# Performance work log

Measured on AMD Instinct MI355X. Metric: run time of the kernel, lower is better.

## Reference

```python
import jax, jax.numpy as jnp
import numpy as np

PILLAR_WH = np.array([0.16, 0.16], np.float32)
MAX_POINTS = 100
MAX_PILLARS = 12000
MIN_XYZ = np.array([-51.2, -51.2, -5.0], np.float32)
MAX_XYZ = np.array([51.2, 51.2, 3.0], np.float32)
PAD_VALUE = 0.0
NGRID = np.ceil((MAX_XYZ[:2] - MIN_XYZ[:2]) / PILLAR_WH).astype(np.int32)  # [640, 640]
WH_N = (2.0 * PILLAR_WH / (MAX_XYZ[:2] - MIN_XYZ[:2])).astype(np.float32)  # pillar size in normalized coords
MIN_XY_N = (MIN_XYZ[:2] / MAX_XYZ[:2]).astype(np.float32)  # = [-1, -1]


def setup_inputs() -> dict:
    key = jax.random.key(0)
    B, P = 4, 50000
    k1, k2, k3 = jax.random.split(key, 3)
    # x,y restricted to [-8, 8] m so occupied pillars (<=100x100=10000) <= max_pillars,
    # making the torch module's random pillar subsampling a deterministic no-op.
    xy = jax.random.uniform(k1, (B, P, 2), minval=-8.0, maxval=8.0, dtype=jnp.float32)
    z = jax.random.uniform(k2, (B, P, 1), minval=-5.0, maxval=3.0, dtype=jnp.float32)
    r = jax.random.uniform(k3, (B, P, 1), dtype=jnp.float32)
    return {"point_clouds": jnp.concatenate([xy, z, r], axis=-1)}


def _per_sample(pc, pidx):
    # pc: (P, 4) normalized points; pidx: (P,) int32 pillar ids
    P = pc.shape[0]
    u, inv = jnp.unique(pidx, size=MAX_PILLARS, fill_value=-1, return_inverse=True)
    counts = jax.ops.segment_sum(jnp.ones((P,), jnp.int32), inv, num_segments=MAX_PILLARS)
    sums = jax.ops.segment_sum(pc[:, :3], inv, num_segments=MAX_PILLARS)
    mean = sums / jnp.maximum(counts, 1).astype(pc.dtype)[:, None]
    # stable sort points by pillar id; rank = position within pillar
    order = jnp.argsort(inv)
    seg = inv[order]
    pts = pc[order]
    start = jnp.cumsum(counts) - counts  # exclusive prefix of counts
    rank = jnp.arange(P, dtype=jnp.int32) - start[seg]
    in_cap = rank < MAX_POINTS
    flat = jnp.where(in_cap, seg * MAX_POINTS + rank, MAX_PILLARS * MAX_POINTS)  # OOB -> dropped
    buf = jnp.zeros((MAX_PILLARS * MAX_POINTS, 4), pc.dtype).at[flat].set(pts, mode='drop')
    occ = jnp.zeros((MAX_PILLARS * MAX_POINTS,), bool).at[flat].set(True, mode='drop')
    buf = buf.reshape(MAX_PILLARS, MAX_POINTS, 4)
    occ = occ.reshape(MAX_PILLARS, MAX_POINTS)
    ij = jnp.stack([u % NGRID[0], u // NGRID[0]], axis=-1).astype(pc.dtype)
    centers = jnp.asarray(MIN_XY_N) + ij * jnp.asarray(WH_N) + jnp.asarray(WH_N) * 0.5
    feat_c = jnp.abs(buf[..., :3] - mean[:, None, :])  # |xyz - pillar mean|
    feat_p = centers[:, None, :] - buf[..., :2]        # pillar center offset
    out = jnp.concatenate([buf, feat_c, feat_p], axis=-1)  # (max_pillars, max_points, 9)
    out = jnp.where(occ[..., None], out, jnp.asarray(PAD_VALUE, pc.dtype))
    return out, u


def reference(point_clouds):
    pc = point_clouds
    xyz_n = 2.0 * (pc[..., :3] - jnp.asarray(MIN_XYZ)) / jnp.asarray(MAX_XYZ - MIN_XYZ) - 1.0
    pc_n = jnp.concatenate([xyz_n, pc[..., 3:]], axis=-1)
    ij = jnp.minimum(
        jnp.floor((xyz_n[..., :2] - jnp.asarray(MIN_XY_N)) / jnp.asarray(WH_N)),
        jnp.asarray(NGRID, xyz_n.dtype) - 1.0,
    ).astype(jnp.int32)
    pidx = ij[..., 1] * int(NGRID[0]) + ij[..., 0]
    out, pillars = jax.vmap(_per_sample)(pc_n, pidx)
    return out, pillars
```

## Files before the change

### kernel.cpp

```cpp
#include <hip/hip_runtime.h>

#define NB 4
#define GRID_X 640
#define NCELL (GRID_X*GRID_X)
#define NWORD (NCELL/32)
#define MAXPIL 12000
#define MAXPTS 100
#define NBLKA (NWORD/256)

typedef unsigned short u16;
typedef unsigned int   u32;

__device__ __forceinline__ float bf16rt(float f) {
    u32 u = __builtin_bit_cast(u32, f);
    u32 r = ((u + 0x7FFFu + ((u >> 16) & 1u)) >> 16) << 16;
    return __builtin_bit_cast(float, r);
}

__device__ __forceinline__ float opaquef(float x) { asm volatile("" : "+v"(x)); return x; }

#define R102 0.009765625f
#define RWH  320.000030517578125f
__device__ __host__ constexpr float WH_N_C() { return (2.0f*0.16f)/(51.2f-(-51.2f)); }

__device__ __forceinline__ float norm_x(float v) {
    float p = 2.0f*(v + 51.2f) * R102;
    return opaquef(p) - 1.0f;
}
__device__ __forceinline__ float norm_z(float v) {
    float p = 2.0f*(v + 5.0f) * 0.125f;
    return opaquef(p) - 1.0f;
}

__device__ __forceinline__ int cell_of(float xn, float yn) {
    float fx = fminf(fmaxf(floorf((xn + 1.0f) * RWH), 0.0f), 639.0f);
    float fy = fminf(fmaxf(floorf((yn + 1.0f) * RWH), 0.0f), 639.0f);
    return (int)fy * GRID_X + (int)fx;
}

__global__ void k_init(int4* __restrict__ ws4, int nw4,
                       float* __restrict__ pillars_f, int* __restrict__ slotCell, int npil) {
    int i = blockIdx.x*blockDim.x + threadIdx.x;
    if (i < nw4) ws4[i] = make_int4(0,0,0,0);
    if (i < npil) { pillars_f[i] = -1.0f; slotCell[i] = -1; }
}

__global__ void k_mask(const float4* __restrict__ pc, int P,
                       u32* __restrict__ occMask, u32* __restrict__ pidxBuf) {
    int i = blockIdx.x*blockDim.x + threadIdx.x;
    if (i >= NB*P) return;
    float4 pt = pc[i];
    int cell = cell_of(norm_x(pt.x), norm_x(pt.y));
    int b = i / P;
    atomicOr(&occMask[b*NWORD + (cell >> 5)], 1u << (cell & 31));
    pidxBuf[i] = (u32)cell;
}

__global__ void k_scanA(const u32* __restrict__ occMask, int* __restrict__ blockSums) {
    __shared__ int lds[256];
    int blk = blockIdx.x % NBLKA;
    int b   = blockIdx.x / NBLKA;
    int w   = blk*256 + threadIdx.x;
    lds[threadIdx.x] = __popc(occMask[b*NWORD + w]);
    __syncthreads();
    for (int d = 128; d > 0; d >>= 1) {
        if (threadIdx.x < d) lds[threadIdx.x] += lds[threadIdx.x + d];
        __syncthreads();
    }
    if (threadIdx.x == 0) blockSums[b*NBLKA + blk] = lds[0];
}

__global__ __launch_bounds__(256) void k_scanC(const u32* __restrict__ occMask,
                        const int* __restrict__ blockSums,
                        int* __restrict__ wordPrefix, float* __restrict__ pillars_f,
                        int* __restrict__ slotCell) {
    __shared__ int lds[256];
    __shared__ int offs;
    int blk = blockIdx.x % NBLKA;
    int b   = blockIdx.x / NBLKA;
    int tid = threadIdx.x;
    int w   = blk*256 + tid;
    u32 m = occMask[b*NWORD + w];
    int pop = __popc(m);
    lds[tid] = pop;
    if (tid < 64) {
        int v = (tid < blk) ? blockSums[b*NBLKA + tid] : 0;
        for (int msk = 1; msk < 64; msk <<= 1) v += __shfl_xor(v, msk);
        if (tid == 0) offs = v;
    }
    __syncthreads();
    for (int d = 1; d < 256; d <<= 1) {
        int t = (tid >= d) ? lds[tid - d] : 0;
        __syncthreads();
        lds[tid] += t;
        __syncthreads();
    }
    int prefix = offs + lds[tid] - pop;
    wordPrefix[b*NWORD + w] = prefix;
    int wbase = w << 5;
    while (m) {
        int bit = __ffs(m) - 1;
        m &= m - 1;
        if (prefix < MAXPIL) {
            int cell = wbase + bit;
            slotCell[b*MAXPIL + prefix] = cell;
            pillars_f[b*MAXPIL + prefix] = bf16rt((float)cell);
        }
        prefix++;
    }
}

__global__ void k_scatter(int P, const u32* __restrict__ pidxBuf,
                          const u32* __restrict__ occMask, const int* __restrict__ wordPrefix,
                          int* __restrict__ slotCnt, u16* __restrict__ idx16) {
    int i = blockIdx.x*blockDim.x + threadIdx.x;
    if (i >= NB*P) return;
    int b = i / P;
    int p = i - b*P;
    int cell = (int)pidxBuf[i];
    int w = cell >> 5, bit = cell & 31;
    u32 m = occMask[b*NWORD + w];
    int slot = wordPrefix[b*NWORD + w] + __popc(m & ((1u << bit) - 1u));
    if (slot >= MAXPIL) return;
    int g = b*MAXPIL + slot;
    int pos = atomicAdd(&slotCnt[g], 1);
    if (pos < MAXPTS) idx16[(size_t)g*MAXPTS + pos] = (u16)p;
}

__global__ __launch_bounds__(64) void k_write(const float4* __restrict__ pc, int P,
                        const int* __restrict__ slotCell, const int* __restrict__ slotCnt,
                        const u16* __restrict__ idx16, float* __restrict__ out) {
    __shared__ __align__(16) float tile[MAXPTS*9 + 4];
    __shared__ int sIdx[MAXPTS];
    int g = blockIdx.x;
    int lane = threadIdx.x;
    float4* out4 = (float4*)out + (size_t)g*225;
    int u = slotCell[g];
    if (u < 0) {
        float4 z = make_float4(0.f,0.f,0.f,0.f);
        for (int i = lane; i < 225; i += 64) out4[i] = z;
        return;
    }
    int b = g / MAXPIL;
    int ntot = slotCnt[g];
    int n = min(ntot, MAXPTS);
    const u16* lst = idx16 + (size_t)g*MAXPTS;

    for (int j = lane; j < n; j += 64) sIdx[j] = lst[j];
    __syncthreads();

    float ax = 0.f, ay = 0.f, az = 0.f;
    for (int j = lane; j < n; j += 64) {
        float4 pt = pc[b*P + sIdx[j]];
        ax += norm_x(pt.x); ay += norm_x(pt.y); az += norm_z(pt.z);
    }
    for (int msk = 1; msk < 64; msk <<= 1) {
        ax += __shfl_xor(ax, msk);
        ay += __shfl_xor(ay, msk);
        az += __shfl_xor(az, msk);
    }
    float den = (float)max(ntot, 1);
    float mx = ax/den, my = ay/den, mz = az/den;
    const float wh = WH_N_C();
    float cx = -1.0f + (float)(u % GRID_X)*wh + wh*0.5f;
    float cy = -1.0f + (float)(u / GRID_X)*wh + wh*0.5f;

    for (int j = lane; j < n; j += 64) {
        int p = sIdx[j];
        int rk = 0;
        for (int k = 0; k < n; k++) rk += (sIdx[k] < p) ? 1 : 0;
        float4 pt = pc[b*P + p];
        float xn = norm_x(pt.x), yn = norm_x(pt.y), zn = norm_z(pt.z);
        float* e = tile + rk*9;
        e[0] = xn; e[1] = yn; e[2] = zn; e[3] = pt.w;
        e[4] = fabsf(xn - mx); e[5] = fabsf(yn - my); e[6] = fabsf(zn - mz);
        e[7] = cx - xn; e[8] = cy - yn;
    }
    int nd = n*9;
    int nf4 = (nd + 3) >> 2;
    if (lane < nf4*4 - nd) tile[nd + lane] = 0.f;
    __syncthreads();

    float4* t4 = (float4*)tile;
    float4 z = make_float4(0.f,0.f,0.f,0.f);
    for (int i = lane; i < 225; i += 64) out4[i] = (i < nf4) ? t4[i] : z;
}

extern "C" void kernel_launch(void* const* d_in, const int* in_sizes, int n_in,
                              void* d_out, int out_size, void* d_ws, size_t ws_size,
                              hipStream_t stream) {
    const float4* pc = (const float4*)d_in[0];
    int P = in_sizes[0] / (NB*4);
    float* out = (float*)d_out;
    float* pillars_f = out + (size_t)NB*MAXPIL*MAXPTS*9;

    u32* occMask   = (u32*)d_ws;
    int* slotCnt   = (int*)(occMask + NB*NWORD);
    int* wordPrefix= slotCnt + NB*MAXPIL;
    int* slotCell  = wordPrefix + NB*NWORD;
    int* blockSums = slotCell + NB*MAXPIL;
    u32* pidxBuf   = (u32*)(blockSums + 256);
    u16* idx16     = (u16*)(pidxBuf + NB*P);

    const int nWs4 = (NB*NWORD + NB*MAXPIL)/4;
    const int npil = NB*MAXPIL;
    int initThreads = npil > nWs4 ? npil : nWs4;

    k_init<<<(initThreads+255)/256, 256, 0, stream>>>((int4*)occMask, nWs4, pillars_f, slotCell, npil);
    k_mask<<<(NB*P+255)/256, 256, 0, stream>>>(pc, P, occMask, pidxBuf);
    k_scanA<<<NB*NBLKA, 256, 0, stream>>>(occMask, blockSums);
    k_scanC<<<NB*NBLKA, 256, 0, stream>>>(occMask, blockSums, wordPrefix, pillars_f, slotCell);
    k_scatter<<<(NB*P+255)/256, 256, 0, stream>>>(P, pidxBuf, occMask, wordPrefix, slotCnt, idx16);
    k_write<<<NB*MAXPIL, 64, 0, stream>>>(pc, P, slotCell, slotCnt, idx16, out);
}
```

Before: 243.5 us.

## Merge scan kernels and pack four pillars per write block

Replaces the two-pass scan (block sums, then prefix) with one kernel where each block recomputes its offset by popcounting every preceding mask word, which removes a launch and the blockSums buffer. The write kernel now runs four independent wavefronts per 256-thread block, each handling one pillar with its own LDS tile. Because each wavefront only touches its own tile, the __syncthreads barriers are dropped. The merged scan does redundant work that grows with block index (up to about 50 words per thread), and the mean now divides by ntot directly, which is safe only because occupied pillars always hold at least one point.

```diff
diff --git a/kernel.cpp b/kernel.cpp
--- a/kernel.cpp
+++ b/kernel.cpp
@@ -7,6 +7,7 @@
 #define MAXPIL 12000
 #define MAXPTS 100
 #define NBLKA (NWORD/256)
+#define PPB 4
 
 typedef unsigned short u16;
 typedef unsigned int   u32;
@@ -56,48 +57,36 @@
     pidxBuf[i] = (u32)cell;
 }
 
-__global__ void k_scanA(const u32* __restrict__ occMask, int* __restrict__ blockSums) {
-    __shared__ int lds[256];
-    int blk = blockIdx.x % NBLKA;
-    int b   = blockIdx.x / NBLKA;
-    int w   = blk*256 + threadIdx.x;
-    lds[threadIdx.x] = __popc(occMask[b*NWORD + w]);
+__global__ __launch_bounds__(256) void k_scan(const u32* __restrict__ occMask,
+                        int* __restrict__ wordPrefix, float* __restrict__ pillars_f,
+                        int* __restrict__ slotCell) {
+    __shared__ int arr[256];
+    __shared__ int offs_s;
+    int b = blockIdx.x / NBLKA, blk = blockIdx.x % NBLKA, t = threadIdx.x;
+    const u32* msk = occMask + b*NWORD;
+    int acc = 0;
+    for (int w = t; w < blk*256; w += 256) acc += __popc(msk[w]);
+    arr[t] = acc;
     __syncthreads();
     for (int d = 128; d > 0; d >>= 1) {
-        if (threadIdx.x < d) lds[threadIdx.x] += lds[threadIdx.x + d];
+        if (t < d) arr[t] += arr[t + d];
         __syncthreads();
     }
-    if (threadIdx.x == 0) blockSums[b*NBLKA + blk] = lds[0];
-}
-
-__global__ __launch_bounds__(256) void k_scanC(const u32* __restrict__ occMask,
-                        const int* __restrict__ blockSums,
-                        int* __restrict__ wordPrefix, float* __restrict__ pillars_f,
-                        int* __restrict__ slotCell) {
-    __shared__ int lds[256];
-    __shared__ int offs;
-    int blk = blockIdx.x % NBLKA;
-    int b   = blockIdx.x / NBLKA;
-    int tid = threadIdx.x;
-    int w   = blk*256 + tid;
-    u32 m = occMask[b*NWORD + w];
+    if (t == 0) offs_s = arr[0];
+    __syncthreads();
+    u32 m = msk[blk*256 + t];
     int pop = __popc(m);
-    lds[tid] = pop;
-    if (tid < 64) {
-        int v = (tid < blk) ? blockSums[b*NBLKA + tid] : 0;
-        for (int msk = 1; msk < 64; msk <<= 1) v += __shfl_xor(v, msk);
-        if (tid == 0) offs = v;
-    }
+    arr[t] = pop;
     __syncthreads();
     for (int d = 1; d < 256; d <<= 1) {
-        int t = (tid >= d) ? lds[tid - d] : 0;
+        int v = (t >= d) ? arr[t - d] : 0;
         __syncthreads();
-        lds[tid] += t;
+        arr[t] += v;
         __syncthreads();
     }
-    int prefix = offs + lds[tid] - pop;
-    wordPrefix[b*NWORD + w] = prefix;
-    int wbase = w << 5;
+    int prefix = offs_s + arr[t] - pop;
+    wordPrefix[b*NWORD + blk*256 + t] = prefix;
+    int wbase = (blk*256 + t) << 5;
     while (m) {
         int bit = __ffs(m) - 1;
         m &= m - 1;
@@ -106,7 +95,7 @@
             slotCell[b*MAXPIL + prefix] = cell;
             pillars_f[b*MAXPIL + prefix] = bf16rt((float)cell);
         }
-        prefix++;
+        ++prefix;
     }
 }
 
@@ -127,17 +116,18 @@
     if (pos < MAXPTS) idx16[(size_t)g*MAXPTS + pos] = (u16)p;
 }
 
-__global__ __launch_bounds__(64) void k_write(const float4* __restrict__ pc, int P,
+__global__ __launch_bounds__(256, 8) void k_write(const float4* __restrict__ pc, int P,
                         const int* __restrict__ slotCell, const int* __restrict__ slotCnt,
                         const u16* __restrict__ idx16, float* __restrict__ out) {
-    __shared__ __align__(16) float tile[MAXPTS*9 + 4];
-    __shared__ int sIdx[MAXPTS];
-    int g = blockIdx.x;
-    int lane = threadIdx.x;
+    __shared__ __align__(16) float tile[PPB][MAXPTS*9 + 4];
+    __shared__ int sIdx[PPB][MAXPTS];
+    int wv   = threadIdx.x >> 6;
+    int lane = threadIdx.x & 63;
+    int g = blockIdx.x*PPB + wv;
     float4* out4 = (float4*)out + (size_t)g*225;
     int u = slotCell[g];
+    float4 z = make_float4(0.f,0.f,0.f,0.f);
     if (u < 0) {
-        float4 z = make_float4(0.f,0.f,0.f,0.f);
         for (int i = lane; i < 225; i += 64) out4[i] = z;
         return;
     }
@@ -145,44 +135,43 @@
     int ntot = slotCnt[g];
     int n = min(ntot, MAXPTS);
     const u16* lst = idx16 + (size_t)g*MAXPTS;
-
-    for (int j = lane; j < n; j += 64) sIdx[j] = lst[j];
-    __syncthreads();
+    float* mytile = tile[wv];
+    int*   myidx  = sIdx[wv];
+
+    for (int j = lane; j < n; j += 64) myidx[j] = lst[j];
 
     float ax = 0.f, ay = 0.f, az = 0.f;
     for (int j = lane; j < n; j += 64) {
-        float4 pt = pc[b*P + sIdx[j]];
+        float4 pt = pc[(size_t)b*P + myidx[j]];
         ax += norm_x(pt.x); ay += norm_x(pt.y); az += norm_z(pt.z);
     }
-    for (int msk = 1; msk < 64; msk <<= 1) {
-        ax += __shfl_xor(ax, msk);
-        ay += __shfl_xor(ay, msk);
-        az += __shfl_xor(az, msk);
-    }
-    float den = (float)max(ntot, 1);
+    for (int m = 1; m < 64; m <<= 1) {
+        ax += __shfl_xor(ax, m);
+        ay += __shfl_xor(ay, m);
+        az += __shfl_xor(az, m);
+    }
+    float den = (float)ntot;
     float mx = ax/den, my = ay/den, mz = az/den;
     const float wh = WH_N_C();
     float cx = -1.0f + (float)(u % GRID_X)*wh + wh*0.5f;
     float cy = -1.0f + (float)(u / GRID_X)*wh + wh*0.5f;
 
     for (int j = lane; j < n; j += 64) {
-        int p = sIdx[j];
+        int p = myidx[j];
         int rk = 0;
-        for (int k = 0; k < n; k++) rk += (sIdx[k] < p) ? 1 : 0;
-        float4 pt = pc[b*P + p];
+        for (int k = 0; k < n; ++k) rk += (myidx[k] < p) ? 1 : 0;
+        float4 pt = pc[(size_t)b*P + p];
         float xn = norm_x(pt.x), yn = norm_x(pt.y), zn = norm_z(pt.z);
-        float* e = tile + rk*9;
+        float* e = mytile + rk*9;
         e[0] = xn; e[1] = yn; e[2] = zn; e[3] = pt.w;
         e[4] = fabsf(xn - mx); e[5] = fabsf(yn - my); e[6] = fabsf(zn - mz);
         e[7] = cx - xn; e[8] = cy - yn;
     }
     int nd = n*9;
     int nf4 = (nd + 3) >> 2;
-    if (lane < nf4*4 - nd) tile[nd + lane] = 0.f;
-    __syncthreads();
-
-    float4* t4 = (float4*)tile;
-    float4 z = make_float4(0.f,0.f,0.f,0.f);
+    if (lane < nf4*4 - nd) mytile[nd + lane] = 0.f;
+
+    float4* t4 = (float4*)mytile;
     for (int i = lane; i < 225; i += 64) out4[i] = (i < nf4) ? t4[i] : z;
 }
 
@@ -198,8 +187,7 @@
     int* slotCnt   = (int*)(occMask + NB*NWORD);
     int* wordPrefix= slotCnt + NB*MAXPIL;
     int* slotCell  = wordPrefix + NB*NWORD;
-    int* blockSums = slotCell + NB*MAXPIL;
-    u32* pidxBuf   = (u32*)(blockSums + 256);
+    u32* pidxBuf   = (u32*)(slotCell + NB*MAXPIL);
     u16* idx16     = (u16*)(pidxBuf + NB*P);
 
     const int nWs4 = (NB*NWORD + NB*MAXPIL)/4;
@@ -208,8 +196,7 @@
 
     k_init<<<(initThreads+255)/256, 256, 0, stream>>>((int4*)occMask, nWs4, pillars_f, slotCell, npil);
     k_mask<<<(NB*P+255)/256, 256, 0, stream>>>(pc, P, occMask, pidxBuf);
-    k_scanA<<<NB*NBLKA, 256, 0, stream>>>(occMask, blockSums);
-    k_scanC<<<NB*NBLKA, 256, 0, stream>>>(occMask, blockSums, wordPrefix, pillars_f, slotCell);
+    k_scan<<<NB*NBLKA, 256, 0, stream>>>(occMask, wordPrefix, pillars_f, slotCell);
     k_scatter<<<(NB*P+255)/256, 256, 0, stream>>>(P, pidxBuf, occMask, wordPrefix, slotCnt, idx16);
-    k_write<<<NB*MAXPIL, 64, 0, stream>>>(pc, P, slotCell, slotCnt, idx16, out);
-}
+    k_write<<<NB*MAXPIL/PPB, 256, 0, stream>>>(pc, P, slotCell, slotCnt, idx16, out);
+}
```

After: 245.5 us. No clear change (+0.8%).
